# Kernel optimization log

Measured on AMD Instinct MI355X. Metric: run time of the kernel, lower is better.

The kernel has to match this reference:

```python
import jax, jax.numpy as jnp
import numpy as np

HEADS = 8
DIM_HEAD = 64
SCALE = DIM_HEAD ** -0.5
LN_EPS = 1e-5

def setup_inputs() -> dict:
    key = jax.random.key(0)
    k0, k1, k2 = jax.random.split(key, 3)
    B, S, D = 4, 2048, 512
    inner = HEADS * DIM_HEAD
    return {
        "x": jax.random.normal(k0, (B, S, D), dtype=jnp.float32),
        "ln_gamma": jnp.ones((D,), dtype=jnp.float32),
        "ln_beta": jnp.zeros((D,), dtype=jnp.float32),
        "w_qkv": jax.random.normal(k1, (D, 3 * inner), dtype=jnp.float32) * (D ** -0.5),
        "w_out": jax.random.normal(k2, (inner, D), dtype=jnp.float32) * (inner ** -0.5),
        "b_out": jnp.zeros((D,), dtype=jnp.float32),
    }

def reference(x, ln_gamma, ln_beta, w_qkv, w_out, b_out):
    B, S, D = x.shape
    # LayerNorm
    mu = jnp.mean(x, axis=-1, keepdims=True)
    var = jnp.mean(jnp.square(x - mu), axis=-1, keepdims=True)
    xn = (x - mu) * jax.lax.rsqrt(var + LN_EPS) * ln_gamma + ln_beta
    # QKV projection (no bias)
    qkv = xn @ w_qkv  # [B, S, 3*inner]
    q, k, v = jnp.split(qkv, 3, axis=-1)
    def to_heads(t):
        return t.reshape(B, S, HEADS, DIM_HEAD).transpose(0, 2, 1, 3)  # [B,H,S,Dh]
    q, k, v = to_heads(q), to_heads(k), to_heads(v)
    # Naive attention with materialized score matrix
    dots = jnp.einsum("bhsd,bhtd->bhst", q, k) * SCALE
    attn = jax.nn.softmax(dots, axis=-1)
    out = jnp.einsum("bhst,bhtd->bhsd", attn, v)
    out = out.transpose(0, 2, 1, 3).reshape(B, S, HEADS * DIM_HEAD)
    return out @ w_out + b_out
```

## Files before the change

### kernel.cpp

```cpp
#include <hip/hip_runtime.h>
#include <hip/hip_bf16.h>
#include <stdint.h>

typedef __bf16 bf16;
typedef __bf16 bf16x8 __attribute__((ext_vector_type(8)));
typedef __bf16 bf16x4 __attribute__((ext_vector_type(4)));
typedef float  f32x4  __attribute__((ext_vector_type(4)));

#define MFMA16(A, B, C) __builtin_amdgcn_mfma_f32_16x16x32_bf16((A), (B), (C), 0, 0, 0)

static constexpr int Bsz = 4, Seq = 2048, Dm = 512, Hh = 8, Dh = 64;

__device__ __forceinline__ void g2l_16(void* lds, const void* gp) {
  __builtin_amdgcn_global_load_lds((__attribute__((address_space(1))) void*)gp,
                                   (__attribute__((address_space(3))) void*)lds, 16, 0, 0);
}

__device__ __forceinline__ float max3f(float a, float b, float c) {
  return fmaxf(fmaxf(a, b), c);
}

__global__ __launch_bounds__(256) void ln_cast_kernel(
    const float* __restrict__ x, const float* __restrict__ g,
    const float* __restrict__ be, bf16* __restrict__ xn) {
  const int row  = blockIdx.x * 4 + (threadIdx.x >> 6);
  const int lane = threadIdx.x & 63;
  const f32x4* xr = (const f32x4*)(x + (size_t)row * Dm);
  f32x4 v0 = xr[lane];
  f32x4 v1 = xr[lane + 64];
  float s = (v0.x + v0.y + v0.z + v0.w) + (v1.x + v1.y + v1.z + v1.w);
#pragma unroll
  for (int off = 32; off > 0; off >>= 1) s += __shfl_xor(s, off);
  const float mu = s * (1.0f / Dm);
  f32x4 d0 = v0 - mu, d1 = v1 - mu;
  float q = d0.x * d0.x + d0.y * d0.y + d0.z * d0.z + d0.w * d0.w
          + d1.x * d1.x + d1.y * d1.y + d1.z * d1.z + d1.w * d1.w;
#pragma unroll
  for (int off = 32; off > 0; off >>= 1) q += __shfl_xor(q, off);
  const float rs = rsqrtf(q * (1.0f / Dm) + 1e-5f);
  const f32x4* gr = (const f32x4*)g;
  const f32x4* br = (const f32x4*)be;
  f32x4 g0 = gr[lane], g1 = gr[lane + 64];
  f32x4 b0 = br[lane], b1 = br[lane + 64];
  f32x4 y0 = d0 * rs * g0 + b0;
  f32x4 y1 = d1 * rs * g1 + b1;
  bf16x4 o0 = { (bf16)y0.x, (bf16)y0.y, (bf16)y0.z, (bf16)y0.w };
  bf16x4 o1 = { (bf16)y1.x, (bf16)y1.y, (bf16)y1.z, (bf16)y1.w };
  bf16x4* orow = (bf16x4*)(xn + (size_t)row * Dm);
  orow[lane]      = o0;
  orow[lane + 64] = o1;
}

__global__ __launch_bounds__(256) void tcast_kernel(
    const float* __restrict__ src, bf16* __restrict__ dst, int R, int C,
    int qrows, float qscale) {
  __shared__ float t[32][33];
  const int c0 = blockIdx.x * 32, r0 = blockIdx.y * 32;
  const int tx = threadIdx.x & 31, ty = threadIdx.x >> 5;
#pragma unroll
  for (int i = 0; i < 32; i += 8)
    t[ty + i][tx] = src[(size_t)(r0 + ty + i) * C + c0 + tx];
  __syncthreads();
#pragma unroll
  for (int i = 0; i < 32; i += 8) {
    const int rr = c0 + ty + i;
    const float sc = rr < qrows ? qscale : 1.0f;
    dst[(size_t)rr * R + r0 + tx] = (bf16)(t[tx][ty + i] * sc);
  }
}

__global__ __launch_bounds__(256) void gemm_qkv_kernel(
    const bf16* __restrict__ A,
    const bf16* __restrict__ Bt,
    bf16* __restrict__ Qb, bf16* __restrict__ Kb, bf16* __restrict__ VT) {
  constexpr int K = 512;
  __shared__ __align__(16) bf16 As[128 * 32];
  __shared__ __align__(16) bf16 Bs[128 * 32];
  const int m0 = blockIdx.x * 128, n0 = blockIdx.y * 128;
  const int tid = threadIdx.x, lane = tid & 63, wave = tid >> 6;
  const int lr = lane & 15, lg = lane >> 4;
  const int wm = (wave >> 1) * 64, wn = (wave & 1) * 64;
  const int srow = wave * 16 + (lane >> 2);
  const int scol = (lane & 3) * 8;
  const bf16* ga = A  + (size_t)(m0 + srow) * K + scol;
  const bf16* gb = Bt + (size_t)(n0 + srow) * K + scol;
  bf16* lA = As + wave * 512;
  bf16* lB = Bs + wave * 512;
  f32x4 acc[4][4] = {};
  for (int k0 = 0; k0 < K; k0 += 32) {
    g2l_16(lA,        ga + k0);
    g2l_16(lA + 2048, ga + (size_t)64 * K + k0);
    g2l_16(lB,        gb + k0);
    g2l_16(lB + 2048, gb + (size_t)64 * K + k0);
    asm volatile("s_waitcnt vmcnt(0)" ::: "memory");
    __syncthreads();
    bf16x8 af[4], bfr[4];
#pragma unroll
    for (int i = 0; i < 4; ++i)
      af[i] = *(const bf16x8*)&As[(wm + i * 16 + lr) * 32 + lg * 8];
#pragma unroll
    for (int j = 0; j < 4; ++j)
      bfr[j] = *(const bf16x8*)&Bs[(wn + j * 16 + lr) * 32 + lg * 8];
#pragma unroll
    for (int i = 0; i < 4; ++i)
#pragma unroll
      for (int j = 0; j < 4; ++j)
        acc[i][j] = MFMA16(af[i], bfr[j], acc[i][j]);
    __syncthreads();
  }
#pragma unroll
  for (int j = 0; j < 4; ++j) {
    const int n = n0 + wn + j * 16 + lr;
    const int which = n >> 9, h = (n >> 6) & 7, dh = n & 63;
    if (which < 2) {
      bf16* dst = which == 0 ? Qb : Kb;
#pragma unroll
      for (int i = 0; i < 4; ++i)
#pragma unroll
        for (int r = 0; r < 4; ++r) {
          const int m = m0 + wm + i * 16 + lg * 4 + r;
          const int b = m >> 11, s2 = m & 2047;
          dst[((size_t)((b * Hh + h) * Seq + s2) << 6) | dh] = (bf16)acc[i][j][r];
        }
    } else {
#pragma unroll
      for (int i = 0; i < 4; ++i)
#pragma unroll
        for (int r = 0; r < 4; ++r) {
          const int m = m0 + wm + i * 16 + lg * 4 + r;
          const int b = m >> 11, s2 = m & 2047;
          VT[((size_t)((b * Hh + h) * Dh + dh)) * Seq + s2] = (bf16)acc[i][j][r];
        }
    }
  }
}

__global__ __launch_bounds__(256) void gemm_out_kernel(
    const bf16* __restrict__ A,
    const bf16* __restrict__ Bt,
    const float* __restrict__ bias, float* __restrict__ out) {
  constexpr int K = 512;
  __shared__ __align__(16) bf16 As[128 * 32];
  __shared__ __align__(16) bf16 Bs[128 * 32];
  const int m0 = blockIdx.x * 128, n0 = blockIdx.y * 128;
  const int tid = threadIdx.x, lane = tid & 63, wave = tid >> 6;
  const int lr = lane & 15, lg = lane >> 4;
  const int wm = (wave >> 1) * 64, wn = (wave & 1) * 64;
  const int srow = wave * 16 + (lane >> 2);
  const int scol = (lane & 3) * 8;
  const bf16* ga = A  + (size_t)(m0 + srow) * K + scol;
  const bf16* gb = Bt + (size_t)(n0 + srow) * K + scol;
  bf16* lA = As + wave * 512;
  bf16* lB = Bs + wave * 512;
  f32x4 acc[4][4] = {};
  for (int k0 = 0; k0 < K; k0 += 32) {
    g2l_16(lA,        ga + k0);
    g2l_16(lA + 2048, ga + (size_t)64 * K + k0);
    g2l_16(lB,        gb + k0);
    g2l_16(lB + 2048, gb + (size_t)64 * K + k0);
    asm volatile("s_waitcnt vmcnt(0)" ::: "memory");
    __syncthreads();
    bf16x8 af[4], bfr[4];
#pragma unroll
    for (int i = 0; i < 4; ++i)
      af[i] = *(const bf16x8*)&As[(wm + i * 16 + lr) * 32 + lg * 8];
#pragma unroll
    for (int j = 0; j < 4; ++j)
      bfr[j] = *(const bf16x8*)&Bs[(wn + j * 16 + lr) * 32 + lg * 8];
#pragma unroll
    for (int i = 0; i < 4; ++i)
#pragma unroll
      for (int j = 0; j < 4; ++j)
        acc[i][j] = MFMA16(af[i], bfr[j], acc[i][j]);
    __syncthreads();
  }
#pragma unroll
  for (int j = 0; j < 4; ++j) {
    const int n = n0 + wn + j * 16 + lr;
    const float bv = bias[n];
#pragma unroll
    for (int i = 0; i < 4; ++i)
#pragma unroll
      for (int r = 0; r < 4; ++r) {
        const int m = m0 + wm + i * 16 + lg * 4 + r;
        out[(size_t)m * 512 + n] = acc[i][j][r] + bv;
      }
  }
}

__global__ __launch_bounds__(256) void attn6_kernel(
    const bf16* __restrict__ Qb, const bf16* __restrict__ Kb,
    const bf16* __restrict__ VT, bf16* __restrict__ A2) {
  const int o   = blockIdx.x + gridDim.x * blockIdx.y;
  const int nid = ((o & 7) << 6) + (o >> 3);
  const int qc = nid & 15, bh = nid >> 4;
  const int b = bh >> 3, h = bh & 7;
  const int tid = threadIdx.x, lane = tid & 63, wave = tid >> 6;
  const int lr = lane & 15, lg = lane >> 4;
  const int q0 = qc * 128 + wave * 32;
  const bf16* Qh = Qb + (size_t)bh * Seq * Dh;
  const bf16* Kh = Kb + (size_t)bh * Seq * Dh;
  const bf16* Vh = VT + (size_t)bh * Dh * Seq;

  __shared__ __align__(16) bf16 KV[2][8192];
  __shared__ __align__(16) bf16 Pl[4][2][16][72];

  const int xs   = lr & 7;
  const int col0 = (lg ^ xs) * 8;
  const bf16* kv = &KV[0][0];
  const int kb0 = lr * 64 + col0;
  const int kb1 = lr * 64 + (col0 ^ 32);
  bf16* pw0 = &Pl[wave][0][lr][lg * 4];
  bf16* pw1 = &Pl[wave][1][lr][lg * 4];
  const bf16* pr0 = &Pl[wave][0][lr][lg * 8];
  const bf16* pr1 = &Pl[wave][1][lr][lg * 8];

  const int krow = tid >> 3;
  const int kc   = (((tid & 7) ^ (krow & 7)) * 8);
  const bf16* gK = Kh + (size_t)krow * 64 + kc;
  const bf16* gV = Vh + (size_t)krow * Seq + kc;
  bf16* ldsD = &KV[0][0] + tid * 8;

  bf16x8 qf[2][2];
#pragma unroll
  for (int qb = 0; qb < 2; ++qb) {
    qf[qb][0] = *(const bf16x8*)&Qh[(size_t)(q0 + qb * 16 + lr) * 64 + lg * 8];
    qf[qb][1] = *(const bf16x8*)&Qh[(size_t)(q0 + qb * 16 + lr) * 64 + 32 + lg * 8];
  }

  f32x4 oa[2][4] = {};
  f32x4 ol[2] = {};
  float m[2] = { -1e30f, -1e30f };
  bf16x8 ones;
#pragma unroll
  for (int i = 0; i < 8; ++i) ones[i] = (bf16)1.0f;

  auto STAGE = [&](int dstOff, int t0) {
    g2l_16(ldsD + dstOff,        gK + (size_t)t0 * 64);
    g2l_16(ldsD + dstOff + 2048, gK + (size_t)t0 * 64 + 2048);
    g2l_16(ldsD + dstOff + 4096, gV + t0);
    g2l_16(ldsD + dstOff + 6144, gV + (size_t)32 * Seq + t0);
  };

  auto TILE = [&](int buf) {
    const int kB = buf * 8192;
    f32x4 st[2][4] = {};
    __builtin_amdgcn_s_setprio(1);
#pragma unroll
    for (int c = 0; c < 4; ++c) {
      bf16x8 kf0 = *(const bf16x8*)&kv[kb0 + kB + c * 1024];
      bf16x8 kf1 = *(const bf16x8*)&kv[kb1 + kB + c * 1024];
      st[0][c] = MFMA16(kf0, qf[0][0], st[0][c]);
      st[0][c] = MFMA16(kf1, qf[0][1], st[0][c]);
      st[1][c] = MFMA16(kf0, qf[1][0], st[1][c]);
      st[1][c] = MFMA16(kf1, qf[1][1], st[1][c]);
    }
    __builtin_amdgcn_s_setprio(0);
#pragma unroll
    for (int qb = 0; qb < 2; ++qb) {
      float m0 = max3f(st[qb][0][0], st[qb][0][1], st[qb][0][2]);
      float m1 = max3f(st[qb][0][3], st[qb][1][0], st[qb][1][1]);
      float m2 = max3f(st[qb][1][2], st[qb][1][3], st[qb][2][0]);
      float m3 = max3f(st[qb][2][1], st[qb][2][2], st[qb][2][3]);
      float m4 = max3f(st[qb][3][0], st[qb][3][1], st[qb][3][2]);
      float mx = max3f(max3f(m0, m1, m2), m3, fmaxf(m4, st[qb][3][3]));
      mx = fmaxf(mx, __shfl_xor(mx, 16));
      mx = fmaxf(mx, __shfl_xor(mx, 32));
      if (__any(mx > m[qb] + 3.0f)) {
        const float mn = fmaxf(m[qb], mx);
        const float al = exp2f(m[qb] - mn);
        m[qb] = mn;
#pragma unroll
        for (int j = 0; j < 4; ++j) {
          const float aj = __shfl(al, lg * 4 + j);
          ol[qb][j] *= aj;
#pragma unroll
          for (int n = 0; n < 4; ++n) oa[qb][n][j] *= aj;
        }
      }
      bf16* pw = qb ? pw1 : pw0;
#pragma unroll
      for (int c = 0; c < 4; ++c) {
        bf16x4 pk;
#pragma unroll
        for (int j = 0; j < 4; ++j) pk[j] = (bf16)exp2f(st[qb][c][j] - m[qb]);
        *(bf16x4*)&pw[c * 16] = pk;
      }
    }
    bf16x8 pf[2][2];
    pf[0][0] = *(const bf16x8*)&pr0[0];
    pf[0][1] = *(const bf16x8*)&pr0[32];
    pf[1][0] = *(const bf16x8*)&pr1[0];
    pf[1][1] = *(const bf16x8*)&pr1[32];
    __builtin_amdgcn_s_setprio(1);
    ol[0] = MFMA16(pf[0][0], ones, ol[0]);
    ol[0] = MFMA16(pf[0][1], ones, ol[0]);
    ol[1] = MFMA16(pf[1][0], ones, ol[1]);
    ol[1] = MFMA16(pf[1][1], ones, ol[1]);
#pragma unroll
    for (int n = 0; n < 4; ++n) {
      bf16x8 vf0 = *(const bf16x8*)&kv[kb0 + kB + 4096 + n * 1024];
      bf16x8 vf1 = *(const bf16x8*)&kv[kb1 + kB + 4096 + n * 1024];
      oa[0][n] = MFMA16(pf[0][0], vf0, oa[0][n]);
      oa[0][n] = MFMA16(pf[0][1], vf1, oa[0][n]);
      oa[1][n] = MFMA16(pf[1][0], vf0, oa[1][n]);
      oa[1][n] = MFMA16(pf[1][1], vf1, oa[1][n]);
    }
    __builtin_amdgcn_s_setprio(0);
  };

  STAGE(0, 0);
  asm volatile("s_waitcnt vmcnt(0)" ::: "memory");
  __syncthreads();

  for (int it = 0; it < 16; ++it) {
    const int t0 = it * 128;
    STAGE(8192, t0 + 64);
    TILE(0);
    asm volatile("s_waitcnt vmcnt(0)" ::: "memory");
    __syncthreads();
    if (it < 15) STAGE(0, t0 + 128);
    TILE(1);
    asm volatile("s_waitcnt vmcnt(0)" ::: "memory");
    __syncthreads();
  }

#pragma unroll
  for (int qb = 0; qb < 2; ++qb) {
#pragma unroll
    for (int j = 0; j < 4; ++j) {
      const float lj = 1.0f / ol[qb][j];
      const int s2 = q0 + qb * 16 + lg * 4 + j;
#pragma unroll
      for (int n = 0; n < 4; ++n)
        A2[(size_t)(b * Seq + s2) * 512 + h * 64 + n * 16 + lr] = (bf16)(oa[qb][n][j] * lj);
    }
  }
}

extern "C" void kernel_launch(void* const* d_in, const int* in_sizes, int n_in,
                              void* d_out, int out_size, void* d_ws, size_t ws_size,
                              hipStream_t stream) {
  const float* x    = (const float*)d_in[0];
  const float* gam  = (const float*)d_in[1];
  const float* bet  = (const float*)d_in[2];
  const float* wqkv = (const float*)d_in[3];
  const float* wout = (const float*)d_in[4];
  const float* bout = (const float*)d_in[5];
  float* out = (float*)d_out;

  bf16* xn    = (bf16*)d_ws;
  bf16* wqkvT = xn    + (size_t)8192 * 512;
  bf16* woutT = wqkvT + (size_t)1536 * 512;
  bf16* Qb    = woutT + (size_t)512 * 512;
  bf16* Kb    = Qb    + (size_t)4 * 8 * 2048 * 64;
  bf16* VT    = Kb    + (size_t)4 * 8 * 2048 * 64;
  bf16* A2    = xn;

  const float K1 = 0.18033688011112042f;

  ln_cast_kernel<<<2048, 256, 0, stream>>>(x, gam, bet, xn);
  tcast_kernel<<<dim3(48, 16), 256, 0, stream>>>(wqkv, wqkvT, 512, 1536, 512, K1);
  tcast_kernel<<<dim3(16, 16), 256, 0, stream>>>(wout, woutT, 512, 512, 0, 1.0f);
  gemm_qkv_kernel<<<dim3(64, 12), 256, 0, stream>>>(xn, wqkvT, Qb, Kb, VT);
  attn6_kernel<<<dim3(16, 32), 256, 0, stream>>>(Qb, Kb, VT, A2);
  gemm_out_kernel<<<dim3(64, 4), 256, 0, stream>>>(A2, woutT, bout, out);
}
```

Baseline: 117.3 us.

## Switch attention kernel to 32x32x16 MFMA tiles with reorganized P layout

Result: faster. 114.5 us (-2.4%).

```diff
diff --git a/kernel.cpp b/kernel.cpp
--- a/kernel.cpp
+++ b/kernel.cpp
@@ -6,8 +6,10 @@
 typedef __bf16 bf16x8 __attribute__((ext_vector_type(8)));
 typedef __bf16 bf16x4 __attribute__((ext_vector_type(4)));
 typedef float  f32x4  __attribute__((ext_vector_type(4)));
+typedef float  f32x16 __attribute__((ext_vector_type(16)));
 
 #define MFMA16(A, B, C) __builtin_amdgcn_mfma_f32_16x16x32_bf16((A), (B), (C), 0, 0, 0)
+#define MFMA32(A, B, C) __builtin_amdgcn_mfma_f32_32x32x16_bf16((A), (B), (C), 0, 0, 0)
 
 static constexpr int Bsz = 4, Seq = 2048, Dm = 512, Hh = 8, Dh = 64;
 
@@ -188,7 +190,7 @@
   }
 }
 
-__global__ __launch_bounds__(256) void attn6_kernel(
+__global__ __launch_bounds__(256) void attn7_kernel(
     const bf16* __restrict__ Qb, const bf16* __restrict__ Kb,
     const bf16* __restrict__ VT, bf16* __restrict__ A2) {
   const int o   = blockIdx.x + gridDim.x * blockIdx.y;
@@ -196,44 +198,24 @@
   const int qc = nid & 15, bh = nid >> 4;
   const int b = bh >> 3, h = bh & 7;
   const int tid = threadIdx.x, lane = tid & 63, wave = tid >> 6;
-  const int lr = lane & 15, lg = lane >> 4;
-  const int q0 = qc * 128 + wave * 32;
+  const int q_l = lane & 31, h5 = lane >> 5;
+  const int kx  = q_l & 7;
+  const int q0w = qc * 128 + wave * 32;
   const bf16* Qh = Qb + (size_t)bh * Seq * Dh;
   const bf16* Kh = Kb + (size_t)bh * Seq * Dh;
   const bf16* Vh = VT + (size_t)bh * Dh * Seq;
 
   __shared__ __align__(16) bf16 KV[2][8192];
-  __shared__ __align__(16) bf16 Pl[4][2][16][72];
-
-  const int xs   = lr & 7;
-  const int col0 = (lg ^ xs) * 8;
+  __shared__ __align__(16) bf16 Pl[4][32 * 64];
+
   const bf16* kv = &KV[0][0];
-  const int kb0 = lr * 64 + col0;
-  const int kb1 = lr * 64 + (col0 ^ 32);
-  bf16* pw0 = &Pl[wave][0][lr][lg * 4];
-  bf16* pw1 = &Pl[wave][1][lr][lg * 4];
-  const bf16* pr0 = &Pl[wave][0][lr][lg * 8];
-  const bf16* pr1 = &Pl[wave][1][lr][lg * 8];
+  bf16* Pw = &Pl[wave][q_l * 64];
 
   const int krow = tid >> 3;
   const int kc   = (((tid & 7) ^ (krow & 7)) * 8);
   const bf16* gK = Kh + (size_t)krow * 64 + kc;
   const bf16* gV = Vh + (size_t)krow * Seq + kc;
   bf16* ldsD = &KV[0][0] + tid * 8;
-
-  bf16x8 qf[2][2];
-#pragma unroll
-  for (int qb = 0; qb < 2; ++qb) {
-    qf[qb][0] = *(const bf16x8*)&Qh[(size_t)(q0 + qb * 16 + lr) * 64 + lg * 8];
-    qf[qb][1] = *(const bf16x8*)&Qh[(size_t)(q0 + qb * 16 + lr) * 64 + 32 + lg * 8];
-  }
-
-  f32x4 oa[2][4] = {};
-  f32x4 ol[2] = {};
-  float m[2] = { -1e30f, -1e30f };
-  bf16x8 ones;
-#pragma unroll
-  for (int i = 0; i < 8; ++i) ones[i] = (bf16)1.0f;
 
   auto STAGE = [&](int dstOff, int t0) {
     g2l_16(ldsD + dstOff,        gK + (size_t)t0 * 64);
@@ -242,69 +224,75 @@
     g2l_16(ldsD + dstOff + 6144, gV + (size_t)32 * Seq + t0);
   };
 
+  bf16x8 qfr[4];
+#pragma unroll
+  for (int s = 0; s < 4; ++s)
+    qfr[s] = *(const bf16x8*)&Qh[(size_t)(q0w + q_l) * 64 + 16 * s + 8 * h5];
+
+  f32x16 oa0 = {}, oa1 = {}, ol = {};
+  float m = -1e30f;
+  bf16x8 ones;
+#pragma unroll
+  for (int i = 0; i < 8; ++i) ones[i] = (bf16)1.0f;
+
   auto TILE = [&](int buf) {
     const int kB = buf * 8192;
-    f32x4 st[2][4] = {};
+    f32x16 st0 = {}, st1 = {};
     __builtin_amdgcn_s_setprio(1);
 #pragma unroll
-    for (int c = 0; c < 4; ++c) {
-      bf16x8 kf0 = *(const bf16x8*)&kv[kb0 + kB + c * 1024];
-      bf16x8 kf1 = *(const bf16x8*)&kv[kb1 + kB + c * 1024];
-      st[0][c] = MFMA16(kf0, qf[0][0], st[0][c]);
-      st[0][c] = MFMA16(kf1, qf[0][1], st[0][c]);
-      st[1][c] = MFMA16(kf0, qf[1][0], st[1][c]);
-      st[1][c] = MFMA16(kf1, qf[1][1], st[1][c]);
+    for (int s = 0; s < 4; ++s) {
+      const int eoff = ((2 * s + h5) ^ kx) << 3;
+      bf16x8 kf0 = *(const bf16x8*)&kv[kB + q_l * 64 + eoff];
+      bf16x8 kf1 = *(const bf16x8*)&kv[kB + (32 + q_l) * 64 + eoff];
+      st0 = MFMA32(kf0, qfr[s], st0);
+      st1 = MFMA32(kf1, qfr[s], st1);
     }
     __builtin_amdgcn_s_setprio(0);
-#pragma unroll
-    for (int qb = 0; qb < 2; ++qb) {
-      float m0 = max3f(st[qb][0][0], st[qb][0][1], st[qb][0][2]);
-      float m1 = max3f(st[qb][0][3], st[qb][1][0], st[qb][1][1]);
-      float m2 = max3f(st[qb][1][2], st[qb][1][3], st[qb][2][0]);
-      float m3 = max3f(st[qb][2][1], st[qb][2][2], st[qb][2][3]);
-      float m4 = max3f(st[qb][3][0], st[qb][3][1], st[qb][3][2]);
-      float mx = max3f(max3f(m0, m1, m2), m3, fmaxf(m4, st[qb][3][3]));
-      mx = fmaxf(mx, __shfl_xor(mx, 16));
-      mx = fmaxf(mx, __shfl_xor(mx, 32));
-      if (__any(mx > m[qb] + 3.0f)) {
-        const float mn = fmaxf(m[qb], mx);
-        const float al = exp2f(m[qb] - mn);
-        m[qb] = mn;
-#pragma unroll
-        for (int j = 0; j < 4; ++j) {
-          const float aj = __shfl(al, lg * 4 + j);
-          ol[qb][j] *= aj;
-#pragma unroll
-          for (int n = 0; n < 4; ++n) oa[qb][n][j] *= aj;
-        }
+    float mx = max3f(st0[0], st0[1], st1[0]);
+#pragma unroll
+    for (int r = 1; r < 8; ++r) mx = max3f(st0[2 * r], st0[2 * r + 1], mx);
+#pragma unroll
+    for (int r = 0; r < 5; ++r) mx = max3f(st1[2 * r + 1], st1[2 * r + 2], mx);
+    mx = max3f(st1[11], st1[12], mx);
+    mx = max3f(st1[13], st1[14], mx);
+    mx = fmaxf(st1[15], mx);
+    mx = fmaxf(mx, __shfl_xor(mx, 32));
+    if (__any(mx > m + 3.0f)) {
+      const float mn = fmaxf(m, mx);
+      const float al = exp2f(m - mn);
+      m = mn;
+#pragma unroll
+      for (int r = 0; r < 16; ++r) {
+        const int qr = (r & 3) + 8 * (r >> 2) + 4 * h5;
+        const float aj = __shfl(al, qr);
+        ol[r] *= aj; oa0[r] *= aj; oa1[r] *= aj;
       }
-      bf16* pw = qb ? pw1 : pw0;
-#pragma unroll
-      for (int c = 0; c < 4; ++c) {
-        bf16x4 pk;
-#pragma unroll
-        for (int j = 0; j < 4; ++j) pk[j] = (bf16)exp2f(st[qb][c][j] - m[qb]);
-        *(bf16x4*)&pw[c * 16] = pk;
+    }
+#pragma unroll
+    for (int t = 0; t < 4; ++t) {
+      bf16x4 p0, p1;
+#pragma unroll
+      for (int j = 0; j < 4; ++j) {
+        p0[j] = (bf16)exp2f(st0[4 * t + j] - m);
+        p1[j] = (bf16)exp2f(st1[4 * t + j] - m);
       }
-    }
-    bf16x8 pf[2][2];
-    pf[0][0] = *(const bf16x8*)&pr0[0];
-    pf[0][1] = *(const bf16x8*)&pr0[32];
-    pf[1][0] = *(const bf16x8*)&pr1[0];
-    pf[1][1] = *(const bf16x8*)&pr1[32];
+      *(bf16x4*)&Pw[((t ^ kx) << 3) + 4 * h5]       = p0;
+      *(bf16x4*)&Pw[(((t + 4) ^ kx) << 3) + 4 * h5] = p1;
+    }
+    bf16x8 pa[4];
+#pragma unroll
+    for (int s = 0; s < 4; ++s)
+      pa[s] = *(const bf16x8*)&Pw[((2 * s + h5) ^ kx) << 3];
     __builtin_amdgcn_s_setprio(1);
-    ol[0] = MFMA16(pf[0][0], ones, ol[0]);
-    ol[0] = MFMA16(pf[0][1], ones, ol[0]);
-    ol[1] = MFMA16(pf[1][0], ones, ol[1]);
-    ol[1] = MFMA16(pf[1][1], ones, ol[1]);
-#pragma unroll
-    for (int n = 0; n < 4; ++n) {
-      bf16x8 vf0 = *(const bf16x8*)&kv[kb0 + kB + 4096 + n * 1024];
-      bf16x8 vf1 = *(const bf16x8*)&kv[kb1 + kB + 4096 + n * 1024];
-      oa[0][n] = MFMA16(pf[0][0], vf0, oa[0][n]);
-      oa[0][n] = MFMA16(pf[0][1], vf1, oa[0][n]);
-      oa[1][n] = MFMA16(pf[1][0], vf0, oa[1][n]);
-      oa[1][n] = MFMA16(pf[1][1], vf1, oa[1][n]);
+#pragma unroll
+    for (int s = 0; s < 4; ++s) ol = MFMA32(pa[s], ones, ol);
+#pragma unroll
+    for (int s = 0; s < 4; ++s) {
+      const int eoff = ((2 * s + h5) ^ kx) << 3;
+      bf16x8 vf0 = *(const bf16x8*)&kv[kB + 4096 + q_l * 64 + eoff];
+      bf16x8 vf1 = *(const bf16x8*)&kv[kB + 4096 + (32 + q_l) * 64 + eoff];
+      oa0 = MFMA32(pa[s], vf0, oa0);
+      oa1 = MFMA32(pa[s], vf1, oa1);
     }
     __builtin_amdgcn_s_setprio(0);
   };
@@ -326,15 +314,12 @@
   }
 
 #pragma unroll
-  for (int qb = 0; qb < 2; ++qb) {
-#pragma unroll
-    for (int j = 0; j < 4; ++j) {
-      const float lj = 1.0f / ol[qb][j];
-      const int s2 = q0 + qb * 16 + lg * 4 + j;
-#pragma unroll
-      for (int n = 0; n < 4; ++n)
-        A2[(size_t)(b * Seq + s2) * 512 + h * 64 + n * 16 + lr] = (bf16)(oa[qb][n][j] * lj);
-    }
+  for (int r = 0; r < 16; ++r) {
+    const int qr = (r & 3) + 8 * (r >> 2) + 4 * h5;
+    const float inv = 1.0f / ol[r];
+    const size_t rowb = (size_t)(b * Seq + q0w + qr) * 512 + h * 64;
+    A2[rowb + q_l]      = (bf16)(oa0[r] * inv);
+    A2[rowb + 32 + q_l] = (bf16)(oa1[r] * inv);
   }
 }
 
@@ -363,6 +348,6 @@
   tcast_kernel<<<dim3(48, 16), 256, 0, stream>>>(wqkv, wqkvT, 512, 1536, 512, K1);
   tcast_kernel<<<dim3(16, 16), 256, 0, stream>>>(wout, woutT, 512, 512, 0, 1.0f);
   gemm_qkv_kernel<<<dim3(64, 12), 256, 0, stream>>>(xn, wqkvT, Qb, Kb, VT);
-  attn6_kernel<<<dim3(16, 32), 256, 0, stream>>>(Qb, Kb, VT, A2);
+  attn7_kernel<<<dim3(16, 32), 256, 0, stream>>>(Qb, Kb, VT, A2);
   gemm_out_kernel<<<dim3(64, 4), 256, 0, stream>>>(A2, woutT, bout, out);
 }
```
